# Kernel optimization log

Measured on AMD Instinct MI355X. Metric: run time of the kernel, lower is better.

The kernel has to match this reference:

```python
import jax, jax.numpy as jnp
import numpy as np

NMS_THR = 0.5
PULL_W = 1.0
PUSH_W = 1.0
EPS = 1e-6


def _pairwise_iou(b1, b2):
    # mmdet-style IoU with the +1 pixel convention. b1: [M,4], b2: [N,4] -> [M,N]
    lt = jnp.maximum(b1[:, None, :2], b2[None, :, :2])
    rb = jnp.minimum(b1[:, None, 2:], b2[None, :, 2:])
    wh = jnp.clip(rb - lt + 1.0, 0.0)
    overlap = wh[..., 0] * wh[..., 1]
    a1 = (b1[:, 2] - b1[:, 0] + 1.0) * (b1[:, 3] - b1[:, 1] + 1.0)
    a2 = (b2[:, 2] - b2[:, 0] + 1.0) * (b2[:, 3] - b2[:, 1] + 1.0)
    return overlap / (a1[:, None] + a2[None, :] - overlap)


def _single_img(gt_inds, gt_box, props):
    # gt_inds: [N] int32 (>=0 positive, <0 ignore), gt_box: [G,4], props: [N,5]
    N = props.shape[0]
    G = gt_box.shape[0]
    pos = gt_inds >= 0
    boxes = props[:, :4]
    scores = props[:, 4]
    # push_select=True: rows of the IoU matrix are detached, columns carry grad
    iou = _pairwise_iou(jax.lax.stop_gradient(boxes), boxes)
    gt_iou = _pairwise_iou(gt_box, gt_box)
    safe_g = jnp.maximum(gt_inds, 0)
    score_key = jax.lax.stop_gradient(scores)
    NEG = jnp.float32(-1e30)

    def step(carry, _):
        alive, rec, tpull, tpush, pcnt, qcnt = carry
        any_alive = jnp.any(alive)
        i = jnp.argmax(jnp.where(alive, score_key, NEG))  # pop highest score
        g = safe_g[i]
        alive_p = alive.at[i].set(False)
        # pull: toward the recorded max-score box of the same gt
        has_rec = rec[g] >= 0
        rec_i = jnp.maximum(rec[g], 0)
        ms_iou = jnp.maximum(iou[i, rec_i], EPS)
        pull = -jnp.log(ms_iou) * scores[i]  # pull_relax=False, use_score=True
        # push: overlapping survivors assigned to a different gt, whose IoU
        # with i exceeds the gt-gt IoU
        row = iou[i]
        overlap = alive_p & (row > NMS_THR)
        final = overlap & (gt_inds != g) & (row > gt_iou[g, safe_g])
        cnt = jnp.sum(final)
        safe_row = jnp.where(final, row, 0.0)
        lj = -jnp.log(1.0 + NMS_THR - safe_row) * score_key  # push_relax=True, score detached
        push = jnp.where(cnt > 0,
                         jnp.sum(jnp.where(final, lj, 0.0)) / jnp.maximum(cnt, 1).astype(row.dtype),
                         0.0)
        remaining = jnp.any(alive_p)
        add = any_alive & remaining  # torch breaks BEFORE accumulating when idx empties
        tpull = tpull + jnp.where(add & has_rec, pull, 0.0)
        tpush = tpush + jnp.where(add, push, 0.0)
        pcnt = pcnt + jnp.where(any_alive & has_rec, 1, 0)  # counted even on the break step
        qcnt = qcnt + jnp.where(add, cnt, 0)
        new_rec = jnp.where(any_alive & ~has_rec, rec.at[g].set(i.astype(jnp.int32)), rec)
        new_alive = jnp.where(any_alive, alive_p & ~overlap, alive)
        return (new_alive, new_rec, tpull, tpush, pcnt, qcnt), None

    init = (pos, jnp.full((G,), -1, jnp.int32), jnp.float32(0.0), jnp.float32(0.0),
            jnp.int32(0), jnp.int32(0))
    (alive, rec, tpull, tpush, pcnt, qcnt), _ = jax.lax.scan(step, init, None, length=N)
    valid = (jnp.sum(pos) > 1).astype(jnp.float32)  # <=1 positive -> zero loss
    pull_loss = tpull / (pcnt.astype(jnp.float32) + EPS) * valid
    push_loss = tpush / (qcnt.astype(jnp.float32) + EPS) * valid
    return push_loss, pull_loss


def _make_boxes(key, shape):
    xy = jax.random.uniform(key, shape[:-1] + (2,)) * 800.0
    wh = jax.random.uniform(jax.random.fold_in(key, 1), shape[:-1] + (2,)) * 200.0 + 8.0
    return jnp.concatenate([xy, xy + wh], axis=-1)


def setup_inputs() -> dict:
    key = jax.random.key(0)
    B, N, G = 4, 2048, 64
    k0, k1, k2, k3 = jax.random.split(key, 4)
    boxes = _make_boxes(k0, (B, N, 4))
    scores = jax.random.uniform(k1, (B, N, 1))
    proposal_list = jnp.concatenate([boxes, scores], axis=-1)
    gt_bboxes = _make_boxes(k2, (B, G, 4))
    anchor_gt_inds = jax.random.randint(k3, (B, N), 0, G, dtype=jnp.int32)
    return {
        "gt_inds": anchor_gt_inds,  # ignored: single_nms_loss overwrites it
        "anchor_gt_inds": anchor_gt_inds,
        "gt_bboxes": gt_bboxes,
        "proposal_list": proposal_list,
    }


def reference(gt_inds, anchor_gt_inds, gt_bboxes, proposal_list):
    push, pull = jax.vmap(_single_img)(anchor_gt_inds, gt_bboxes, proposal_list)
    push_loss = jnp.mean(push) * PUSH_W
    pull_loss = jnp.mean(pull) * PULL_W
    return jnp.stack([push_loss, pull_loss])  # [nms_push_loss, nms_pull_loss]
```

## Files before the change

### kernel.cpp

```cpp
#include <hip/hip_runtime.h>

#define NN 2048
#define GG 64
#define TS 128
#define NT (NN / TS)
#define NPAIR (NT * (NT + 1) / 2)
#define MAXE 14336
#define CAPBLK 2048
#define STH 1024
#define NWAVE (STH / 64)

typedef unsigned long long u64;
typedef unsigned short u16;
typedef unsigned int u32;

__device__ __forceinline__ float iou4(float4 a, float4 b) {
    float w = fminf(a.z, b.z) - fmaxf(a.x, b.x) + 1.0f;
    float h = fminf(a.w, b.w) - fmaxf(a.y, b.y) + 1.0f;
    w = fmaxf(w, 0.0f);
    h = fmaxf(h, 0.0f);
    float ov = w * h;
    float aa = (a.z - a.x + 1.0f) * (a.w - a.y + 1.0f);
    float ab = (b.z - b.x + 1.0f) * (b.w - b.y + 1.0f);
    return ov / (aa + ab - ov);
}

__device__ __forceinline__ float wredf(float v) {
    for (int o = 32; o > 0; o >>= 1) v += __shfl_down(v, o);
    return v;
}
__device__ __forceinline__ int wredi(int v) {
    for (int o = 32; o > 0; o >>= 1) v += __shfl_down(v, o);
    return v;
}
__device__ __forceinline__ u64 wredmin64(u64 v) {
    for (int o = 32; o > 0; o >>= 1) {
        u64 w = __shfl_down(v, o);
        v = (w < v) ? w : v;
    }
    return v;
}

__device__ __forceinline__ bool earlier(u32 sa, int a, u32 sb, int b) {
    return (sa > sb) || (sa == sb && a < b);
}
__device__ __forceinline__ u64 make_key(u32 sbits, int j) {
    return ((u64)sbits << 32) | (u64)(NN - 1 - j);
}
__device__ __forceinline__ float4 load_box(const float* pb, int j) {
    return make_float4(pb[j * 5 + 0], pb[j * 5 + 1], pb[j * 5 + 2], pb[j * 5 + 3]);
}

__global__ __launch_bounds__(256) void pair_kernel(const int* __restrict__ gt_inds,
                                                   const float* __restrict__ props,
                                                   int* __restrict__ counts, u32* __restrict__ edges,
                                                   float4* __restrict__ sbox, u32* __restrict__ sscB,
                                                   int* __restrict__ sgt,
                                                   float* __restrict__ acc, u32* __restrict__ ctr2) {
    const int im = blockIdx.x / NPAIR;
    const int p = blockIdx.x % NPAIR;
    int q = p;
    int ta = 0;
    while (q >= NT - ta) { q -= NT - ta; ++ta; }
    const int tb = ta + q;
    const float* pb = props + (size_t)im * NN * 5;
    const int* gbi = gt_inds + (size_t)im * NN;
    const int base = im * NN;

    __shared__ float4 Abox[TS], Bbox[TS];
    __shared__ u32 Asc[TS], Bsc[TS];
    __shared__ int Ag[TS], Bg[TS];
    __shared__ u32 ebuf[CAPBLK];
    __shared__ int lcnt;
    const int tid = threadIdx.x;
    if (tid == 0) lcnt = 0;
    if (blockIdx.x == 0 && tid == 0) { acc[0] = 0.f; acc[1] = 0.f; *ctr2 = 0u; }

    for (int t = tid; t < 2 * TS; t += 256) {
        int half = t >> 7, r = t & (TS - 1);
        int j = (half ? tb : ta) * TS + r;
        float4 bxv = load_box(pb, j);
        u32 sb = __float_as_uint(pb[j * 5 + 4]);
        int g = gbi[j];
        if (half == 0) { Abox[r] = bxv; Asc[r] = sb; Ag[r] = g; }
        else           { Bbox[r] = bxv; Bsc[r] = sb; Bg[r] = g; }
    }
    __syncthreads();

    if (ta == tb && tid < TS) {
        sbox[base + ta * TS + tid] = Abox[tid];
        sscB[base + ta * TS + tid] = Asc[tid];
        sgt[base + ta * TS + tid] = Ag[tid];
    }

    const int pr = tid & (TS - 1);
    const int half = tid >> 7;
    const float4 rb = Abox[pr];
    const u32 rs = Asc[pr];
    const int i = ta * TS + pr;
    if (Ag[pr] >= 0) {
        #pragma unroll 4
        for (int k = 0; k < TS / 2; ++k) {
            int jl = half * (TS / 2) + k;
            if (ta == tb && jl <= pr) continue;
            if (Bg[jl] < 0) continue;
            float v = iou4(rb, Bbox[jl]);
            if (v > 0.5f) {
                int j = tb * TS + jl;
                int late, early;
                if (earlier(rs, i, Bsc[jl], j)) { late = j; early = i; }
                else                            { late = i; early = j; }
                int slot = atomicAdd(&lcnt, 1);
                if (slot < CAPBLK) ebuf[slot] = ((u32)late << 16) | (u32)early;
            }
        }
    }
    __syncthreads();
    const int n = min(lcnt, CAPBLK);
    if (tid == 0) counts[blockIdx.x] = n;
    u32* ge = edges + (size_t)blockIdx.x * CAPBLK;
    for (int e = tid; e < n; e += 256) ge[e] = ebuf[e];
}

union SumWl {
    float sumA[NN];
    u16 wl[2][NN];
};

__global__ __launch_bounds__(STH) void scan_kernel(const float* __restrict__ gt_boxes,
                                                   const float4* __restrict__ sbox,
                                                   const u32* __restrict__ sscB,
                                                   const int* __restrict__ sgt,
                                                   const int* __restrict__ counts, const u32* __restrict__ edges,
                                                   float* __restrict__ acc, u32* __restrict__ ctr2,
                                                   float* __restrict__ out, int B) {
    __shared__ float4 bx[NN];
    __shared__ u32 scoreL[NN];
    __shared__ SumWl u;
    __shared__ int cw[NN];
    __shared__ u16 eoff[NN + 2];
    __shared__ u16 ent[MAXE];
    __shared__ unsigned char st[NN];
    __shared__ unsigned char hk[NN];
    __shared__ signed char gtL[NN];
    __shared__ int rcnt[NPAIR];
    __shared__ float4 gtb[GG];
    __shared__ float4 recbox[GG];
    __shared__ u64 firstk[GG];
    __shared__ int wtot[NWAVE];
    __shared__ int s_cnt[2];
    __shared__ u64 s_minkey;
    __shared__ int s_pos, s_qcnt, s_pcnt;
    __shared__ float s_tpush, s_tpull;

    const int im = blockIdx.x, tid = threadIdx.x;
    const int lane = tid & 63, wid = tid >> 6;
    const int base = im * NN;
    volatile unsigned char* vst = st;

    if (tid == 0) {
        s_pos = 0; s_qcnt = 0; s_pcnt = 0; s_tpush = 0.f; s_tpull = 0.f; s_minkey = ~0ull;
        s_cnt[0] = 0; s_cnt[1] = 0;
    }
    if (tid < GG) {
        firstk[tid] = 0ull;
        gtb[tid] = ((const float4*)(gt_boxes + (size_t)im * GG * 4))[tid];
    }
    if (tid < NPAIR) rcnt[tid] = counts[im * NPAIR + tid];

    int lpos = 0;
    for (int j = tid; j < NN; j += STH) {
        bx[j] = sbox[base + j];
        scoreL[j] = sscB[base + j];
        int g = sgt[base + j];
        gtL[j] = (signed char)((g < 0) ? -1 : g);
        st[j] = (g >= 0) ? 0 : 2;
        lpos += (g >= 0) ? 1 : 0;
        cw[j] = 0; hk[j] = 0;
    }
    lpos = wredi(lpos);
    if (lane == 0 && lpos) atomicAdd(&s_pos, lpos);
    __syncthreads();

    for (int r = wid; r < NPAIR; r += NWAVE) {
        int cr = rcnt[r];
        const u32* ge = edges + (size_t)(im * NPAIR + r) * CAPBLK;
        for (int e = lane; e < cr; e += 64) atomicAdd(&cw[ge[e] >> 16], 1);
    }
    __syncthreads();
    {
        int j0 = tid * 2;
        int c0 = cw[j0], c1 = cw[j0 + 1];
        int s = c0 + c1;
        int incl = s;
        for (int o = 1; o < 64; o <<= 1) {
            int v = __shfl_up(incl, o);
            if (lane >= o) incl += v;
        }
        if (lane == 63) wtot[wid] = incl;
        __syncthreads();
        int wpre = 0;
        for (int wq = 0; wq < wid; ++wq) wpre += wtot[wq];
        int excl = wpre + incl - s;
        eoff[j0] = (u16)excl;
        eoff[j0 + 1] = (u16)(excl + c0);
        if (tid == STH - 1) eoff[NN] = (u16)(excl + s);
        cw[j0] = excl;
        cw[j0 + 1] = excl + c0;
    }
    __syncthreads();
    for (int r = wid; r < NPAIR; r += NWAVE) {
        int cr = rcnt[r];
        const u32* ge = edges + (size_t)(im * NPAIR + r) * CAPBLK;
        for (int e = lane; e < cr; e += 64) {
            u32 x = ge[e];
            int pos = atomicAdd(&cw[x >> 16], 1);
            ent[pos] = (u16)(x & 0xffffu);
        }
    }
    __syncthreads();

    for (int j = tid; j < NN; j += STH) {
        if (st[j] != 0) continue;
        int e0 = eoff[j], e1 = eoff[j + 1];
        bool anyK = false, anyU = false;
        for (int e = e0; e < e1; ++e) {
            unsigned char s = vst[ent[e]];
            anyK |= (s == 1);
            anyU |= (s == 0);
        }
        if (anyK) st[j] = 2;
        else if (!anyU) st[j] = 1;
        else { int pos = atomicAdd(&s_cnt[0], 1); u.wl[0][pos] = (u16)j; }
    }
    __syncthreads();

    int src = 0;
    int nwl = s_cnt[0];
    while (nwl > 0) {
        #pragma unroll
        for (int r = 0; r < 2; ++r) {
            for (int w = tid; w < nwl; w += STH) {
                int j = u.wl[src][w];
                if (st[j] != 0) continue;
                int e0 = eoff[j], e1 = eoff[j + 1];
                bool anyK = false, anyU = false;
                for (int e = e0; e < e1; ++e) {
                    unsigned char s = vst[ent[e]];
                    anyK |= (s == 1);
                    anyU |= (s == 0);
                }
                if (anyK) st[j] = 2;
                else if (!anyU) st[j] = 1;
            }
        }
        for (int w = tid; w < nwl; w += STH) {
            int j = u.wl[src][w];
            if (st[j] != 0) continue;
            int e0 = eoff[j], e1 = eoff[j + 1];
            bool anyK = false, anyU = false;
            for (int e = e0; e < e1; ++e) {
                unsigned char s = vst[ent[e]];
                anyK |= (s == 1);
                anyU |= (s == 0);
            }
            if (anyK) st[j] = 2;
            else if (!anyU) st[j] = 1;
            else { int pos = atomicAdd(&s_cnt[src ^ 1], 1); u.wl[src ^ 1][pos] = (u16)j; }
        }
        __syncthreads();
        nwl = s_cnt[src ^ 1];
        if (tid == 0) s_cnt[src] = 0;
        src ^= 1;
        __syncthreads();
    }

    u64 lmin = ~0ull;
    for (int j = tid; j < NN; j += STH) {
        u.sumA[j] = 0.f; cw[j] = 0;
        if (st[j] == 1) {
            u64 kj = make_key(scoreL[j], j);
            if (kj < lmin) lmin = kj;
            atomicMax(&firstk[gtL[j]], kj);
        }
    }
    lmin = wredmin64(lmin);
    if (lane == 0 && lmin != ~0ull) atomicMin(&s_minkey, lmin);
    __syncthreads();

    if (tid < GG) {
        u64 fk = firstk[tid];
        if (fk) recbox[tid] = bx[(NN - 1) - (int)(fk & 0xffffffffu)];
    }

    for (int j = tid; j < NN; j += STH) {
        int g = gtL[j];
        if (st[j] != 2 || g < 0) continue;
        int e0 = eoff[j], e1 = eoff[j + 1];
        int ki = -1; u32 ks = 0;
        for (int e = e0; e < e1; ++e) {
            int ii = ent[e];
            if (st[ii] == 1 && (ki < 0 || earlier(scoreL[ii], ii, ks, ki))) { ki = ii; ks = scoreL[ii]; }
        }
        if (ki < 0) continue;
        hk[ki] = 1;
        float v = iou4(bx[ki], bx[j]);
        int gi = gtL[ki];
        if (g != gi && v > iou4(gtb[gi], gtb[g])) {
            atomicAdd(&cw[ki], 1);
            atomicAdd(&u.sumA[ki], -logf(1.5f - v) * __uint_as_float(scoreL[j]));
        }
    }
    __syncthreads();

    float ltpush = 0.f, ltpull = 0.f;
    int lqcnt = 0, lpcnt = 0;
    const u64 minkey = s_minkey;
    for (int i = tid; i < NN; i += STH) {
        if (st[i] != 1) continue;
        int g = gtL[i];
        u64 ky = make_key(scoreL[i], i);
        u64 fk = firstk[g];
        bool add = (ky != minkey) || (hk[i] != 0);
        int c = cw[i];
        bool hr = fk > ky;
        if (add && c > 0) ltpush += u.sumA[i] / (float)c;
        if (add) lqcnt += c;
        if (hr) ++lpcnt;
        if (add && hr) {
            float v = iou4(bx[i], recbox[g]);
            ltpull += -logf(fmaxf(v, 1e-6f)) * __uint_as_float(scoreL[i]);
        }
    }
    ltpush = wredf(ltpush); ltpull = wredf(ltpull);
    lqcnt = wredi(lqcnt); lpcnt = wredi(lpcnt);
    if (lane == 0) {
        if (ltpush != 0.f) atomicAdd(&s_tpush, ltpush);
        if (ltpull != 0.f) atomicAdd(&s_tpull, ltpull);
        if (lqcnt) atomicAdd(&s_qcnt, lqcnt);
        if (lpcnt) atomicAdd(&s_pcnt, lpcnt);
    }
    __syncthreads();

    if (tid == 0) {
        float valid = (s_pos > 1) ? 1.0f : 0.0f;
        float push_b = s_tpush / ((float)s_qcnt + 1e-6f) * valid;
        float pull_b = s_tpull / ((float)s_pcnt + 1e-6f) * valid;
        atomicAdd(&acc[0], push_b);
        atomicAdd(&acc[1], pull_b);
        __threadfence();
        u32 old = atomicAdd(ctr2, 1u);
        if (old == (u32)(B - 1)) {
            float ps = atomicAdd(&acc[0], 0.0f);
            float pl = atomicAdd(&acc[1], 0.0f);
            float inv = 1.0f / (float)B;
            out[0] = ps * inv * 1.0f;
            out[1] = pl * inv * 1.0f;
        }
    }
}

extern "C" void kernel_launch(void* const* d_in, const int* in_sizes, int n_in,
                              void* d_out, int out_size, void* d_ws, size_t ws_size,
                              hipStream_t stream) {
    const int B = in_sizes[0] / NN;
    const int* anchor_gt = (const int*)d_in[1];
    const float* gtb = (const float*)d_in[2];
    const float* props = (const float*)d_in[3];

    char* w = (char*)d_ws;
    float* acc = (float*)w;
    u32* ctr2 = (u32*)(w + 8);
    size_t o = 128;
    int* counts = (int*)(w + o);   o += ((size_t)B * NPAIR * 4 + 127) & ~(size_t)127;
    float4* sbox = (float4*)(w + o); o += (size_t)B * NN * 16;
    u32* sscB = (u32*)(w + o);     o += (size_t)B * NN * 4;
    int* sgt = (int*)(w + o);      o += (size_t)B * NN * 4;
    u32* edges = (u32*)(w + o);

    pair_kernel<<<dim3(B * NPAIR), dim3(256), 0, stream>>>(anchor_gt, props, counts, edges,
                                                           sbox, sscB, sgt, acc, ctr2);
    scan_kernel<<<dim3(B), dim3(STH), 0, stream>>>(gtb, sbox, sscB, sgt, counts, edges,
                                                   acc, ctr2, (float*)d_out, B);
}
```

Before: 48.71 us.

## Run worklist NMS resolution in a single wavefront with ballot compaction

Moves the iterative worklist loop that resolves keep/suppress status onto one 64-lane wavefront. Worklist compaction now uses ballot/popcount instead of shared atomics, which removes the block-wide barriers that ran every round. The other 15 waves sit idle during this phase, so a long worklist gets far less parallelism. Because each pass now reads statuses that were just updated, it may also need fewer rounds.

Measured after the change: 57.01 us. 17.1% more time.

```diff
diff --git a/kernel.cpp b/kernel.cpp
--- a/kernel.cpp
+++ b/kernel.cpp
@@ -148,7 +148,7 @@
     __shared__ float4 recbox[GG];
     __shared__ u64 firstk[GG];
     __shared__ int wtot[NWAVE];
-    __shared__ int s_cnt[2];
+    __shared__ int s_cnt;
     __shared__ u64 s_minkey;
     __shared__ int s_pos, s_qcnt, s_pcnt;
     __shared__ float s_tpush, s_tpull;
@@ -160,7 +160,7 @@
 
     if (tid == 0) {
         s_pos = 0; s_qcnt = 0; s_pcnt = 0; s_tpush = 0.f; s_tpull = 0.f; s_minkey = ~0ull;
-        s_cnt[0] = 0; s_cnt[1] = 0;
+        s_cnt = 0;
     }
     if (tid < GG) {
         firstk[tid] = 0ull;
@@ -231,49 +231,48 @@
         }
         if (anyK) st[j] = 2;
         else if (!anyU) st[j] = 1;
-        else { int pos = atomicAdd(&s_cnt[0], 1); u.wl[0][pos] = (u16)j; }
-    }
-    __syncthreads();
-
-    int src = 0;
-    int nwl = s_cnt[0];
-    while (nwl > 0) {
-        #pragma unroll
-        for (int r = 0; r < 2; ++r) {
-            for (int w = tid; w < nwl; w += STH) {
-                int j = u.wl[src][w];
-                if (st[j] != 0) continue;
-                int e0 = eoff[j], e1 = eoff[j + 1];
-                bool anyK = false, anyU = false;
-                for (int e = e0; e < e1; ++e) {
-                    unsigned char s = vst[ent[e]];
-                    anyK |= (s == 1);
-                    anyU |= (s == 0);
+        else { int pos = atomicAdd(&s_cnt, 1); u.wl[0][pos] = (u16)j; }
+    }
+    __syncthreads();
+
+    if (wid == 0) {
+        int nwl = s_cnt;
+        int src = 0;
+        while (nwl > 0) {
+            int dst = src ^ 1;
+            int nnew = 0;
+            int nt = (nwl + 63) >> 6;
+            for (int t = 0; t < nt; ++t) {
+                int w = t * 64 + lane;
+                bool keep = false;
+                int j = 0;
+                if (w < nwl) {
+                    j = u.wl[src][w];
+                    if (st[j] == 0) {
+                        int e0 = eoff[j], e1 = eoff[j + 1];
+                        bool anyK = false, anyU = false;
+                        for (int e = e0; e < e1; ++e) {
+                            unsigned char s = vst[ent[e]];
+                            anyK |= (s == 1);
+                            anyU |= (s == 0);
+                        }
+                        if (anyK) st[j] = 2;
+                        else if (!anyU) st[j] = 1;
+                        else keep = true;
+                    }
                 }
-                if (anyK) st[j] = 2;
-                else if (!anyU) st[j] = 1;
+                u64 m = __ballot(keep);
+                if (keep) {
+                    int pos = __popcll(m & ((1ull << lane) - 1ull));
+                    u.wl[dst][nnew + pos] = (u16)j;
+                }
+                nnew += __popcll(m);
             }
-        }
-        for (int w = tid; w < nwl; w += STH) {
-            int j = u.wl[src][w];
-            if (st[j] != 0) continue;
-            int e0 = eoff[j], e1 = eoff[j + 1];
-            bool anyK = false, anyU = false;
-            for (int e = e0; e < e1; ++e) {
-                unsigned char s = vst[ent[e]];
-                anyK |= (s == 1);
-                anyU |= (s == 0);
-            }
-            if (anyK) st[j] = 2;
-            else if (!anyU) st[j] = 1;
-            else { int pos = atomicAdd(&s_cnt[src ^ 1], 1); u.wl[src ^ 1][pos] = (u16)j; }
-        }
-        __syncthreads();
-        nwl = s_cnt[src ^ 1];
-        if (tid == 0) s_cnt[src] = 0;
-        src ^= 1;
-        __syncthreads();
-    }
+            nwl = nnew;
+            src = dst;
+        }
+    }
+    __syncthreads();
 
     u64 lmin = ~0ull;
     for (int j = tid; j < NN; j += STH) {
```
